# Optimization experiments

Hardware: AMD Instinct MI355X
Metric: run time of the kernel (lower is better)

Reference implementation:

```python
import jax, jax.numpy as jnp
import numpy as np

B, T, I, H = 64, 1024, 128, 512

def setup_inputs() -> dict:
    key = jax.random.key(0)
    ks = jax.random.split(key, 7)
    s_ih = 1.0 / np.sqrt(H)
    return {
        "x": jax.random.normal(ks[0], (B, T, I), dtype=jnp.float32),
        "W_ih": jax.random.uniform(ks[1], (H, I), minval=-s_ih, maxval=s_ih, dtype=jnp.float32),
        "W_hh": jax.random.uniform(ks[2], (H, H), minval=-s_ih, maxval=s_ih, dtype=jnp.float32),
        "b_ih": jax.random.uniform(ks[3], (H,), minval=-s_ih, maxval=s_ih, dtype=jnp.float32),
        "b_hh": jax.random.uniform(ks[4], (H,), minval=-s_ih, maxval=s_ih, dtype=jnp.float32),
        "fc_w": jax.random.uniform(ks[5], (1, H), minval=-s_ih, maxval=s_ih, dtype=jnp.float32),
        "fc_b": jax.random.uniform(ks[6], (1,), minval=-s_ih, maxval=s_ih, dtype=jnp.float32),
    }

def reference(x, W_ih, W_hh, b_ih, b_hh, fc_w, fc_b):
    # Precompute input projection for all timesteps: [B,T,H]
    xp = jnp.einsum('bti,hi->bth', x, W_ih) + b_ih + b_hh

    def step(h, xp_t):
        # h: [B,H], xp_t: [B,H]
        h_new = jnp.tanh(xp_t + h @ W_hh.T)
        return h_new, None

    h0 = jnp.zeros((B, H), dtype=x.dtype)
    h_last, _ = jax.lax.scan(step, h0, jnp.swapaxes(xp, 0, 1))  # scan over T
    # final linear head: [B,1]
    return h_last @ fc_w.T + fc_b
```

## Files before the change

### kernel.cpp

```cpp
#include <hip/hip_runtime.h>
#include <math.h>

#define B_ 64
#define T_ 1024
#define I_ 128
#define H_ 512

typedef _Float16 h2_t __attribute__((ext_vector_type(2)));
union U32H2 { unsigned u; h2_t h; };

__device__ __forceinline__ float fdot2u(unsigned a, unsigned b, float c) {
    U32H2 ua, ub; ua.u = a; ub.u = b;
    return __builtin_amdgcn_fdot2(ua.h, ub.h, c, false);
}

__device__ __forceinline__ unsigned packh2(float x, float y) {
    U32H2 r; r.h.x = (_Float16)x; r.h.y = (_Float16)y; return r.u;
}

__global__ void prep(const float* __restrict__ wih, const float* __restrict__ whh,
                     const float* __restrict__ bih, const float* __restrict__ bhh,
                     unsigned* __restrict__ wpack, unsigned* __restrict__ wldsg,
                     unsigned* __restrict__ wih2, float* __restrict__ biasv) {
    int e = blockIdx.x * 256 + threadIdx.x;
    if (e < 512 * 192) {
        int tid = e / 192, r = e % 192;
        int j = r / 48, kk2 = r % 48;
        int c = tid >> 7, g = tid & 127;
        int row = (g << 2) + j;
        int col = (c << 7) + (kk2 << 1);
        wpack[e] = packh2(whh[row * H_ + col], whh[row * H_ + col + 1]);
    }
    if (e < 4 * 16 * 512) {
        int c = e >> 13, m = (e >> 9) & 15, col = e & 511;
        int k = (c << 7) + 96 + (m << 1);
        wldsg[e] = packh2(whh[col * H_ + k], whh[col * H_ + k + 1]);
    }
    if (e < 64 * 512) {
        int i2 = e >> 9, h = e & 511;
        wih2[e] = packh2(wih[h * I_ + (i2 << 1)], wih[h * I_ + (i2 << 1) + 1]);
    }
    if (e < H_) biasv[e] = bih[e] + bhh[e];
}

__global__ __launch_bounds__(512, 2) void xp_gemm(
    const float* __restrict__ x, const unsigned* __restrict__ wih2,
    const float* __restrict__ biasv, _Float16* __restrict__ xph) {
    __shared__ unsigned w2[64 * 512];
    __shared__ unsigned x2[32 * 64];
    const int tid = threadIdx.x, b = blockIdx.x, t0 = blockIdx.y * 32;

    #pragma unroll
    for (int q = 0; q < 64; ++q) w2[tid + (q << 9)] = wih2[tid + (q << 9)];
    #pragma unroll
    for (int q = 0; q < 4; ++q) {
        int idx = tid * 4 + q;
        int t = idx >> 6, i2 = idx & 63;
        const float2 xv = *(const float2*)(x + ((size_t)b * T_ + t0 + t) * I_ + (i2 << 1));
        x2[idx] = packh2(xv.x, xv.y);
    }
    __syncthreads();
    const float bias = biasv[tid];
    for (int t = 0; t < 32; ++t) {
        float acc = bias;
        #pragma unroll
        for (int i2 = 0; i2 < 64; ++i2)
            acc = fdot2u(x2[(t << 6) + i2], w2[(i2 << 9) + tid], acc);
        xph[((size_t)b * T_ + t0 + t) * H_ + tid] = (_Float16)acc;
    }
}

__global__ __launch_bounds__(512, 2) void rnn_fused(
    const unsigned* __restrict__ xp2,
    const unsigned* __restrict__ wpack,
    const unsigned* __restrict__ wldsg,
    const float* __restrict__ fcw, const float* __restrict__ fcb,
    float* __restrict__ out) {
    __shared__ unsigned wlds[4 * 16 * 512];
    __shared__ float part[4 * 512];
    __shared__ unsigned h2buf[256];
    __shared__ float wsum[4];

    const int tid = threadIdx.x;
    const int b = blockIdx.x;
    const int c = tid >> 7, g = tid & 127;

    {
        const uint4* src = (const uint4*)wldsg;
        uint4* dst = (uint4*)wlds;
        #pragma unroll
        for (int q = 0; q < 16; ++q) dst[tid + (q << 9)] = src[tid + (q << 9)];
    }
    unsigned wreg[4][48];
    {
        const unsigned* wp = wpack + tid * 192;
        #pragma unroll
        for (int j = 0; j < 4; ++j)
            #pragma unroll
            for (int kk2 = 0; kk2 < 48; ++kk2)
                wreg[j][kk2] = wp[j * 48 + kk2];
    }
    if (tid < 256) h2buf[tid] = 0u;
    __syncthreads();

    const unsigned* xpb = xp2 + (size_t)b * T_ * 256;
    const uint4* wlds4 = (const uint4*)wlds;
    float4* part4 = (float4*)part;
    const float2* part2 = (const float2*)part;
    const int hb = c << 6;

    for (int t = 0; t < T_; ++t) {
        unsigned xpw = 0;
        if (tid < 256) xpw = xpb[t * 256 + tid];

        float a0 = 0.f, a1 = 0.f, a2 = 0.f, a3 = 0.f;
        #pragma unroll
        for (int kk2 = 0; kk2 < 48; ++kk2) {
            unsigned hh = h2buf[hb + kk2];
            a0 = fdot2u(wreg[0][kk2], hh, a0);
            a1 = fdot2u(wreg[1][kk2], hh, a1);
            a2 = fdot2u(wreg[2][kk2], hh, a2);
            a3 = fdot2u(wreg[3][kk2], hh, a3);
        }
        #pragma unroll
        for (int m = 0; m < 16; ++m) {
            unsigned hh = h2buf[hb + 48 + m];
            uint4 w4 = wlds4[((c << 4) + m) * 128 + g];
            a0 = fdot2u(w4.x, hh, a0);
            a1 = fdot2u(w4.y, hh, a1);
            a2 = fdot2u(w4.z, hh, a2);
            a3 = fdot2u(w4.w, hh, a3);
        }
        part4[(c << 7) + g] = make_float4(a0, a1, a2, a3);
        __syncthreads();

        if (tid < 256) {
            float2 s0 = part2[tid];
            float2 s1 = part2[256 + tid];
            float2 s2 = part2[512 + tid];
            float2 s3 = part2[768 + tid];
            U32H2 xu; xu.u = xpw;
            float pre0 = (float)xu.h.x + s0.x + s1.x + s2.x + s3.x;
            float pre1 = (float)xu.h.y + s0.y + s1.y + s2.y + s3.y;
            float e0 = __expf(2.0f * pre0), e1 = __expf(2.0f * pre1);
            float h0 = 1.0f - 2.0f / (e0 + 1.0f);
            float h1 = 1.0f - 2.0f / (e1 + 1.0f);
            h2buf[tid] = packh2(h0, h1);
        }
        __syncthreads();
    }

    float p = 0.f;
    if (tid < 256) {
        U32H2 hu; hu.u = h2buf[tid];
        p = (float)hu.h.x * fcw[tid << 1] + (float)hu.h.y * fcw[(tid << 1) + 1];
    }
    #pragma unroll
    for (int off = 32; off >= 1; off >>= 1) p += __shfl_down(p, off, 64);
    if ((tid & 63) == 0 && tid < 256) wsum[tid >> 6] = p;
    __syncthreads();
    if (tid == 0) out[b] = wsum[0] + wsum[1] + wsum[2] + wsum[3] + fcb[0];
}

extern "C" void kernel_launch(void* const* d_in, const int* in_sizes, int n_in,
                              void* d_out, int out_size, void* d_ws, size_t ws_size,
                              hipStream_t stream) {
    const float* x   = (const float*)d_in[0];
    const float* wih = (const float*)d_in[1];
    const float* whh = (const float*)d_in[2];
    const float* bih = (const float*)d_in[3];
    const float* bhh = (const float*)d_in[4];
    const float* fcw = (const float*)d_in[5];
    const float* fcb = (const float*)d_in[6];
    float* out = (float*)d_out;

    unsigned* xp2   = (unsigned*)d_ws;
    unsigned* wpack = xp2 + 16777216;
    unsigned* wldsg = wpack + 98304;
    unsigned* wih2  = wldsg + 32768;
    float*    biasv = (float*)(wih2 + 32768);

    hipLaunchKernelGGL(prep, dim3(384), dim3(256), 0, stream,
                       wih, whh, bih, bhh, wpack, wldsg, wih2, biasv);
    hipLaunchKernelGGL(xp_gemm, dim3(B_, 32), dim3(512), 0, stream,
                       x, wih2, biasv, (_Float16*)xp2);
    hipLaunchKernelGGL(rnn_fused, dim3(B_), dim3(512), 0, stream,
                       xp2, wpack, wldsg, fcw, fcb, out);
}
```

Before: 1.605 ms.

## Reduce RNN step partials with wavefront shuffles and double-buffer hidden state

Remaps the W_hh partitioning so the four K-chunk partial sums for each output row sit in adjacent lanes of one wavefront, so they are combined with xor shuffles rather than through a shared-memory partial buffer. The hidden state is double-buffered in LDS with a padded stride, which cuts each timestep from two block barriers to one. Weight packing is rearranged so global loads into registers and LDS are coalesced across threads. In exchange, only a quarter of lanes now run the tanh, and the padded h layout has to match the final FC readout.

```diff
diff --git a/kernel.cpp b/kernel.cpp
--- a/kernel.cpp
+++ b/kernel.cpp
@@ -13,7 +13,6 @@
     U32H2 ua, ub; ua.u = a; ub.u = b;
     return __builtin_amdgcn_fdot2(ua.h, ub.h, c, false);
 }
-
 __device__ __forceinline__ unsigned packh2(float x, float y) {
     U32H2 r; r.h.x = (_Float16)x; r.h.y = (_Float16)y; return r.u;
 }
@@ -24,21 +23,23 @@
                      unsigned* __restrict__ wih2, float* __restrict__ biasv) {
     int e = blockIdx.x * 256 + threadIdx.x;
     if (e < 512 * 192) {
-        int tid = e / 192, r = e % 192;
-        int j = r / 48, kk2 = r % 48;
-        int c = tid >> 7, g = tid & 127;
-        int row = (g << 2) + j;
-        int col = (c << 7) + (kk2 << 1);
-        wpack[e] = packh2(whh[row * H_ + col], whh[row * H_ + col + 1]);
+        int idx = e >> 9, tid = e & 511;
+        int r = idx / 48, m = idx % 48;
+        int w = tid >> 6, l = tid & 63, c = l & 3, g = l >> 2;
+        int j = w * 64 + g * 4 + r;
+        int word = 64 * c + m;
+        wpack[e] = packh2(whh[j * H_ + 2 * word], whh[j * H_ + 2 * word + 1]);
     }
-    if (e < 4 * 16 * 512) {
-        int c = e >> 13, m = (e >> 9) & 15, col = e & 511;
-        int k = (c << 7) + 96 + (m << 1);
-        wldsg[e] = packh2(whh[col * H_ + k], whh[col * H_ + k + 1]);
+    if (e < 32768) {
+        int r = e & 3, tid = (e >> 2) & 511, slot = e >> 11;
+        int w = tid >> 6, l = tid & 63, c = l & 3, g = l >> 2;
+        int j = w * 64 + g * 4 + r;
+        int word = 64 * c + 48 + slot;
+        wldsg[e] = packh2(whh[j * H_ + 2 * word], whh[j * H_ + 2 * word + 1]);
     }
     if (e < 64 * 512) {
         int i2 = e >> 9, h = e & 511;
-        wih2[e] = packh2(wih[h * I_ + (i2 << 1)], wih[h * I_ + (i2 << 1) + 1]);
+        wih2[e] = packh2(wih[h * I_ + 2 * i2], wih[h * I_ + 2 * i2 + 1]);
     }
     if (e < H_) biasv[e] = bih[e] + bhh[e];
 }
@@ -75,85 +76,87 @@
     const unsigned* __restrict__ wpack,
     const unsigned* __restrict__ wldsg,
     const float* __restrict__ fcw, const float* __restrict__ fcb,
-    float* __restrict__ out) {
-    __shared__ unsigned wlds[4 * 16 * 512];
-    __shared__ float part[4 * 512];
-    __shared__ unsigned h2buf[256];
-    __shared__ float wsum[4];
+    float* __restrict__ out)
+{
+    __shared__ unsigned wlds[32768];
+    __shared__ unsigned hbuf[576];
+    __shared__ float wsum[8];
 
     const int tid = threadIdx.x;
     const int b = blockIdx.x;
-    const int c = tid >> 7, g = tid & 127;
+    const int w = tid >> 6, l = tid & 63;
+    const int c = l & 3, g = l >> 2;
 
     {
         const uint4* src = (const uint4*)wldsg;
         uint4* dst = (uint4*)wlds;
         #pragma unroll
-        for (int q = 0; q < 16; ++q) dst[tid + (q << 9)] = src[tid + (q << 9)];
+        for (int q = 0; q < 16; ++q) dst[q * 512 + tid] = src[q * 512 + tid];
     }
     unsigned wreg[4][48];
-    {
-        const unsigned* wp = wpack + tid * 192;
+    #pragma unroll
+    for (int r = 0; r < 4; ++r)
         #pragma unroll
-        for (int j = 0; j < 4; ++j)
-            #pragma unroll
-            for (int kk2 = 0; kk2 < 48; ++kk2)
-                wreg[j][kk2] = wp[j * 48 + kk2];
-    }
-    if (tid < 256) h2buf[tid] = 0u;
+        for (int m = 0; m < 48; ++m)
+            wreg[r][m] = wpack[(r * 48 + m) * 512 + tid];
+
+    for (int i = tid; i < 576; i += 512) hbuf[i] = 0u;
     __syncthreads();
 
     const unsigned* xpb = xp2 + (size_t)b * T_ * 256;
-    const uint4* wlds4 = (const uint4*)wlds;
-    float4* part4 = (float4*)part;
-    const float2* part2 = (const float2*)part;
-    const int hb = c << 6;
+    const uint4* wq = ((const uint4*)wlds) + tid;
+    const int W0 = w * 32 + g * 2;
+    const int wrbase = 72 * (w >> 1) + 32 * (w & 1) + 2 * g;
 
     for (int t = 0; t < T_; ++t) {
-        unsigned xpw = 0;
-        if (tid < 256) xpw = xpb[t * 256 + tid];
+        const int pc = (t & 1) * 288;
+        const unsigned* hrd = hbuf + pc + 72 * c;
+
+        uint2 xpw = *(const uint2*)(xpb + t * 256 + W0);
 
         float a0 = 0.f, a1 = 0.f, a2 = 0.f, a3 = 0.f;
         #pragma unroll
-        for (int kk2 = 0; kk2 < 48; ++kk2) {
-            unsigned hh = h2buf[hb + kk2];
-            a0 = fdot2u(wreg[0][kk2], hh, a0);
-            a1 = fdot2u(wreg[1][kk2], hh, a1);
-            a2 = fdot2u(wreg[2][kk2], hh, a2);
-            a3 = fdot2u(wreg[3][kk2], hh, a3);
+        for (int m = 0; m < 48; ++m) {
+            unsigned hh = hrd[m];
+            a0 = fdot2u(wreg[0][m], hh, a0);
+            a1 = fdot2u(wreg[1][m], hh, a1);
+            a2 = fdot2u(wreg[2][m], hh, a2);
+            a3 = fdot2u(wreg[3][m], hh, a3);
         }
         #pragma unroll
-        for (int m = 0; m < 16; ++m) {
-            unsigned hh = h2buf[hb + 48 + m];
-            uint4 w4 = wlds4[((c << 4) + m) * 128 + g];
+        for (int s = 0; s < 16; ++s) {
+            unsigned hh = hrd[48 + s];
+            uint4 w4 = wq[s * 512];
             a0 = fdot2u(w4.x, hh, a0);
             a1 = fdot2u(w4.y, hh, a1);
             a2 = fdot2u(w4.z, hh, a2);
             a3 = fdot2u(w4.w, hh, a3);
         }
-        part4[(c << 7) + g] = make_float4(a0, a1, a2, a3);
-        __syncthreads();
+        a0 += __shfl_xor(a0, 1); a0 += __shfl_xor(a0, 2);
+        a1 += __shfl_xor(a1, 1); a1 += __shfl_xor(a1, 2);
+        a2 += __shfl_xor(a2, 1); a2 += __shfl_xor(a2, 2);
+        a3 += __shfl_xor(a3, 1); a3 += __shfl_xor(a3, 2);
 
-        if (tid < 256) {
-            float2 s0 = part2[tid];
-            float2 s1 = part2[256 + tid];
-            float2 s2 = part2[512 + tid];
-            float2 s3 = part2[768 + tid];
-            U32H2 xu; xu.u = xpw;
-            float pre0 = (float)xu.h.x + s0.x + s1.x + s2.x + s3.x;
-            float pre1 = (float)xu.h.y + s0.y + s1.y + s2.y + s3.y;
-            float e0 = __expf(2.0f * pre0), e1 = __expf(2.0f * pre1);
-            float h0 = 1.0f - 2.0f / (e0 + 1.0f);
-            float h1 = 1.0f - 2.0f / (e1 + 1.0f);
-            h2buf[tid] = packh2(h0, h1);
+        if (c == 0) {
+            U32H2 x0, x1; x0.u = xpw.x; x1.u = xpw.y;
+            float p0 = (float)x0.h.x + a0;
+            float p1 = (float)x0.h.y + a1;
+            float p2 = (float)x1.h.x + a2;
+            float p3 = (float)x1.h.y + a3;
+            float e0 = __expf(2.f * p0), e1 = __expf(2.f * p1);
+            float e2 = __expf(2.f * p2), e3 = __expf(2.f * p3);
+            float h0 = 1.f - 2.f / (e0 + 1.f), h1 = 1.f - 2.f / (e1 + 1.f);
+            float h2v = 1.f - 2.f / (e2 + 1.f), h3 = 1.f - 2.f / (e3 + 1.f);
+            uint2 hw; hw.x = packh2(h0, h1); hw.y = packh2(h2v, h3);
+            *(uint2*)(hbuf + (pc ^ 288) + wrbase) = hw;
         }
         __syncthreads();
     }
 
     float p = 0.f;
     if (tid < 256) {
-        U32H2 hu; hu.u = h2buf[tid];
-        p = (float)hu.h.x * fcw[tid << 1] + (float)hu.h.y * fcw[(tid << 1) + 1];
+        U32H2 hu; hu.u = hbuf[72 * (tid >> 6) + (tid & 63)];
+        p = (float)hu.h.x * fcw[2 * tid] + (float)hu.h.y * fcw[2 * tid + 1];
     }
     #pragma unroll
     for (int off = 32; off >= 1; off >>= 1) p += __shfl_down(p, off, 64);
```

Measured after the change: 1.992 ms. 24.1% more time.
